# Performance work log

Measured on AMD Instinct MI355X. Metric: run time of the kernel, lower is better.

The kernel has to match this reference:

```python
import jax, jax.numpy as jnp
import numpy as np

B, N, D, E, FF_MULT = 2, 1024, 1024, 8, 4
H = D * FF_MULT


def setup_inputs() -> dict:
    key = jax.random.key(0)
    k = jax.random.split(key, 6)
    tokens = jax.random.normal(k[0], (B, N, D), dtype=jnp.float32)
    # uniform(0,1): strictly positive -> every expert processes every token
    dispatch_weights = jax.random.uniform(k[1], (B, N, E), dtype=jnp.float32)
    combine_weights = jax.random.uniform(k[2], (B, N, E), dtype=jnp.float32)
    # per-expert SwiGLU params, stacked on leading expert axis.
    # stored pre-transposed: y = x @ W  (torch Linear weight is [out,in])
    xavier_dh = np.sqrt(2.0 / (D + H))
    Wg = jax.random.normal(k[3], (E, D, H), dtype=jnp.float32) * xavier_dh
    Wv = jax.random.normal(k[4], (E, D, H), dtype=jnp.float32) * xavier_dh
    Wo = jax.random.normal(k[5], (E, H, D), dtype=jnp.float32) * (0.02 * xavier_dh)
    scale = jnp.full((E,), 1.0 / E, dtype=jnp.float32)  # output_scale init 1/E
    return {"tokens": tokens, "dispatch_weights": dispatch_weights,
            "combine_weights": combine_weights, "Wg": Wg, "Wv": Wv,
            "Wo": Wo, "scale": scale}


def reference(tokens, dispatch_weights, combine_weights, Wg, Wv, Wo, scale):
    b, n, d = tokens.shape
    x = tokens.reshape(b * n, d)                      # (T, D)
    disp = dispatch_weights.reshape(b * n, E)         # (T, E)
    comb = combine_weights.reshape(b * n, E)          # (T, E)
    # SwiGLU FFN for all experts at once (dense grouped GEMM)
    gate = jax.nn.gelu(jnp.einsum('td,edh->teh', x, Wg), approximate=False)
    value = jnp.einsum('td,edh->teh', x, Wv)
    expert_out = jnp.einsum('teh,ehd->ted', gate * value, Wo)  # (T, E, D)
    expert_out = expert_out * scale[None, :, None]
    # combine: weight by combine_weights where dispatched (dispatch > 0)
    w = jnp.where(disp > 0, comb, 0.0)                # (T, E)
    output = jnp.einsum('ted,te->td', expert_out, w)
    return output.reshape(b, n, d)
```

## Files before the change

kernel.cpp:

```cpp
#include <hip/hip_runtime.h>
#include <math.h>

#define T_TOK 2048
#define DDIM 1024
#define HDIM 4096
#define NEXP 8
#define NPRIME 8192
#define KTOT (NEXP * HDIM)
#define NSPLIT 4

typedef unsigned short u16;
typedef __attribute__((ext_vector_type(4))) float f32x4;
typedef __attribute__((ext_vector_type(8))) __bf16 bf16x8;
typedef __attribute__((ext_vector_type(8))) unsigned short u16x8;
typedef __attribute__((ext_vector_type(4))) unsigned short u16x4;

__device__ __forceinline__ u16 f2bf(float f) {
  unsigned int u = __builtin_bit_cast(unsigned int, f);
  u += 0x7fffu + ((u >> 16) & 1u);
  return (u16)(u >> 16);
}

__device__ __forceinline__ void stage16(const u16* g, u16* l) {
  __builtin_amdgcn_global_load_lds((__attribute__((address_space(1))) void*)g,
                                   (__attribute__((address_space(3))) void*)l,
                                   16, 0, 0);
}

__global__ void cvt_x_kernel(const float* __restrict__ x, u16* __restrict__ xb) {
  int i = (blockIdx.x * 256 + threadIdx.x) * 8;
  float4 a = *(const float4*)(x + i);
  float4 b = *(const float4*)(x + i + 4);
  u16x8 o;
  o[0] = f2bf(a.x); o[1] = f2bf(a.y); o[2] = f2bf(a.z); o[3] = f2bf(a.w);
  o[4] = f2bf(b.x); o[5] = f2bf(b.y); o[6] = f2bf(b.z); o[7] = f2bf(b.w);
  *(u16x8*)(xb + i) = o;
}

__global__ void transpose_all_kernel(const float* __restrict__ Wg,
                                     const float* __restrict__ Wv,
                                     const float* __restrict__ Wo,
                                     u16* __restrict__ wgvT, u16* __restrict__ woT2) {
  __shared__ float lds[64][65];
  const int bid = blockIdx.x;
  const int e = bid / 3072;
  const int r = bid % 3072;
  const int which = r >> 10;
  const int tt = r & 1023;
  const float* src; int R, C;
  if (which == 2) { src = Wo + (size_t)e * HDIM * DDIM; R = HDIM; C = DDIM; }
  else            { src = (which ? Wv : Wg) + (size_t)e * DDIM * HDIM; R = DDIM; C = HDIM; }
  const int nrt = R >> 6;
  const int r0 = (tt % nrt) << 6, c0 = (tt / nrt) << 6;
  const int tid = threadIdx.x;
#pragma unroll
  for (int i = 0; i < 4; ++i) {
    int f4 = tid + 256 * i;
    int row = f4 >> 4, c4 = (f4 & 15) << 2;
    float4 v = *(const float4*)(src + (size_t)(r0 + row) * C + c0 + c4);
    lds[row][c4] = v.x; lds[row][c4 + 1] = v.y; lds[row][c4 + 2] = v.z; lds[row][c4 + 3] = v.w;
  }
  __syncthreads();
#pragma unroll
  for (int i = 0; i < 4; ++i) {
    int f4 = tid + 256 * i;
    int cc = f4 >> 4, r4 = (f4 & 15) << 2;
    u16x4 o;
    o[0] = f2bf(lds[r4][cc]);     o[1] = f2bf(lds[r4 + 1][cc]);
    o[2] = f2bf(lds[r4 + 2][cc]); o[3] = f2bf(lds[r4 + 3][cc]);
    u16* dst;
    if (which == 2) {
      dst = woT2 + (size_t)(c0 + cc) * KTOT + e * HDIM + r0 + r4;
    } else {
      int h = c0 + cc;
      int rowp = ((h >> 4) << 5) + which * 16 + (h & 15);
      dst = wgvT + (size_t)e * NPRIME * DDIM + (size_t)rowp * DDIM + r0 + r4;
    }
    *(u16x4*)dst = o;
  }
}


__global__ void __launch_bounds__(512, 2)
gemm_gv_kernel(const u16* __restrict__ xb, const u16* __restrict__ wgvT,
               const float* __restrict__ disp, const float* __restrict__ comb,
               const float* __restrict__ scale, u16* __restrict__ h) {
  __shared__ u16 lds[3 * 24576];

  const int bid = blockIdx.x;
  const int wg = (bid & 7) * 512 + (bid >> 3);
  const int e  = wg >> 9;
  const int nt = (wg >> 3) & 63;
  const int mt = wg & 7;

  const int tid = threadIdx.x;
  const int lane = tid & 63;
  const int wave = tid >> 6;
  const int wr = wave >> 1;
  const int wc = wave & 1;
  const int l15 = lane & 15;
  const int lkq = lane >> 4;

  const u16* Ag = xb;
  const u16* Bg = wgvT + (size_t)e * NPRIME * DDIM;
  const int Am0 = mt * 256;
  const int Bn0 = nt * 128;

  const u16* gsrc[6];
  int ldst[6];
#pragma unroll
  for (int i = 0; i < 6; ++i) {
    int c = tid + 512 * i;
    if (c < 2048) { int row = c >> 3, sl = c & 7;
      gsrc[i] = Ag + (size_t)(Am0 + row) * DDIM + ((sl ^ (row & 7)) << 3);
    } else { int cb = c - 2048, row = cb >> 3, sl = cb & 7;
      gsrc[i] = Bg + (size_t)(Bn0 + row) * DDIM + ((sl ^ (row & 7)) << 3);
    }
    ldst[i] = c << 3;
  }
  auto STAGE = [&](int t) {
    const int k0 = t << 6;
    u16* lb = lds + (t % 3) * 24576;
#pragma unroll
    for (int i = 0; i < 6; ++i) stage16(gsrc[i] + k0, lb + ldst[i]);
  };

  f32x4 acc[4][4] = {};
  const int NT = DDIM / 64;

  STAGE(0); STAGE(1);
  asm volatile("s_waitcnt vmcnt(6)" ::: "memory");
  __builtin_amdgcn_s_barrier();

  for (int t = 0; t < NT; ++t) {
    if (t + 2 < NT) STAGE(t + 2);
    const u16* lb = lds + (t % 3) * 24576;
    bf16x8 af[2][4], bf[2][4];
#pragma unroll
    for (int ks = 0; ks < 2; ++ks) {
#pragma unroll
      for (int m = 0; m < 4; ++m) {
        int row = wr * 64 + m * 16 + l15;
        int sl = ((ks << 2) | lkq) ^ (row & 7);
        af[ks][m] = *(const bf16x8*)&lb[row * 64 + (sl << 3)];
      }
#pragma unroll
      for (int n = 0; n < 4; ++n) {
        int row = wc * 64 + n * 16 + l15;
        int sl = ((ks << 2) | lkq) ^ (row & 7);
        bf[ks][n] = *(const bf16x8*)&lb[16384 + row * 64 + (sl << 3)];
      }
    }
    __builtin_amdgcn_s_setprio(1);
#pragma unroll
    for (int ks = 0; ks < 2; ++ks)
#pragma unroll
      for (int m = 0; m < 4; ++m)
#pragma unroll
        for (int n = 0; n < 4; ++n)
          acc[m][n] = __builtin_amdgcn_mfma_f32_16x16x32_bf16(af[ks][m], bf[ks][n], acc[m][n], 0, 0, 0);
    __builtin_amdgcn_s_setprio(0);
    if (t < NT - 1) {
      asm volatile("s_waitcnt lgkmcnt(0)" ::: "memory");
      __builtin_amdgcn_sched_barrier(0);
      if (t + 2 < NT) asm volatile("s_waitcnt vmcnt(6)" ::: "memory");
      else            asm volatile("s_waitcnt vmcnt(0)" ::: "memory");
      __builtin_amdgcn_s_barrier();
    }
  }

  const float s_e = scale[e];
  const int hcb = nt * 64 + wc * 32;
#pragma unroll
  for (int m = 0; m < 4; ++m) {
#pragma unroll
    for (int r = 0; r < 4; ++r) {
      const int t = Am0 + wr * 64 + m * 16 + lkq * 4 + r;
      const float dv = disp[t * NEXP + e];
      const float cv = comb[t * NEXP + e];
      const float s = (dv > 0.0f) ? cv * s_e : 0.0f;
#pragma unroll
      for (int j = 0; j < 2; ++j) {
        const float g = acc[m][2 * j][r];
        const float v = acc[m][2 * j + 1][r];
        const float ge = 0.5f * g * (1.0f + erff(g * 0.70710678f));
        h[(size_t)t * KTOT + e * HDIM + hcb + j * 16 + l15] = f2bf(ge * v * s);
      }
    }
  }
}

__global__ void __launch_bounds__(512, 2)
gemm_out_kernel(const u16* __restrict__ hb, const u16* __restrict__ woT2,
                float* __restrict__ P) {
  __shared__ u16 lds[3 * 24576];

  const int bid = blockIdx.x;
  const int wg = (bid & 7) * 32 + (bid >> 3);
  const int kz = wg >> 6;
  const int nt = (wg >> 3) & 7;
  const int mt = wg & 7;

  const int tid = threadIdx.x;
  const int lane = tid & 63;
  const int wave = tid >> 6;
  const int wr = wave >> 1;
  const int wc = wave & 1;
  const int l15 = lane & 15;
  const int lkq = lane >> 4;

  const int Am0 = mt * 256;
  const int Bn0 = nt * 128;
  const int kbase = kz * (KTOT / NSPLIT);

  const u16* gsrc[6];
  int ldst[6];
#pragma unroll
  for (int i = 0; i < 6; ++i) {
    int c = tid + 512 * i;
    if (c < 2048) { int row = c >> 3, sl = c & 7;
      gsrc[i] = hb + (size_t)(Am0 + row) * KTOT + kbase + ((sl ^ (row & 7)) << 3);
    } else { int cb = c - 2048, row = cb >> 3, sl = cb & 7;
      gsrc[i] = woT2 + (size_t)(Bn0 + row) * KTOT + kbase + ((sl ^ (row & 7)) << 3);
    }
    ldst[i] = c << 3;
  }
  auto STAGE = [&](int t) {
    const int k0 = t << 6;
    u16* lb = lds + (t % 3) * 24576;
#pragma unroll
    for (int i = 0; i < 6; ++i) stage16(gsrc[i] + k0, lb + ldst[i]);
  };

  f32x4 acc[4][4] = {};
  const int NT = (KTOT / NSPLIT) / 64;

  STAGE(0); STAGE(1);
  asm volatile("s_waitcnt vmcnt(6)" ::: "memory");
  __builtin_amdgcn_s_barrier();

  for (int t = 0; t < NT; ++t) {
    if (t + 2 < NT) STAGE(t + 2);
    const u16* lb = lds + (t % 3) * 24576;
    bf16x8 af[2][4], bf[2][4];
#pragma unroll
    for (int ks = 0; ks < 2; ++ks) {
#pragma unroll
      for (int m = 0; m < 4; ++m) {
        int row = wr * 64 + m * 16 + l15;
        int sl = ((ks << 2) | lkq) ^ (row & 7);
        af[ks][m] = *(const bf16x8*)&lb[row * 64 + (sl << 3)];
      }
#pragma unroll
      for (int n = 0; n < 4; ++n) {
        int row = wc * 64 + n * 16 + l15;
        int sl = ((ks << 2) | lkq) ^ (row & 7);
        bf[ks][n] = *(const bf16x8*)&lb[16384 + row * 64 + (sl << 3)];
      }
    }
    __builtin_amdgcn_s_setprio(1);
#pragma unroll
    for (int ks = 0; ks < 2; ++ks)
#pragma unroll
      for (int m = 0; m < 4; ++m)
#pragma unroll
        for (int n = 0; n < 4; ++n)
          acc[m][n] = __builtin_amdgcn_mfma_f32_16x16x32_bf16(af[ks][m], bf[ks][n], acc[m][n], 0, 0, 0);
    __builtin_amdgcn_s_setprio(0);
    if (t < NT - 1) {
      asm volatile("s_waitcnt lgkmcnt(0)" ::: "memory");
      __builtin_amdgcn_sched_barrier(0);
      if (t + 2 < NT) asm volatile("s_waitcnt vmcnt(6)" ::: "memory");
      else            asm volatile("s_waitcnt vmcnt(0)" ::: "memory");
      __builtin_amdgcn_s_barrier();
    }
  }

  float* Pp = P + (size_t)kz * (T_TOK * DDIM);
#pragma unroll
  for (int m = 0; m < 4; ++m) {
#pragma unroll
    for (int r = 0; r < 4; ++r) {
      const int t = Am0 + wr * 64 + m * 16 + lkq * 4 + r;
#pragma unroll
      for (int n = 0; n < 4; ++n)
        Pp[(size_t)t * DDIM + Bn0 + wc * 64 + n * 16 + l15] = acc[m][n][r];
    }
  }
}

__global__ void reduce_out_kernel(const float* __restrict__ P, float* __restrict__ out) {
  int i = blockIdx.x * 256 + threadIdx.x;
  float4 a = ((const float4*)P)[i];
#pragma unroll
  for (int s = 1; s < NSPLIT; ++s) {
    float4 b = ((const float4*)P)[i + s * (T_TOK * DDIM / 4)];
    a.x += b.x; a.y += b.y; a.z += b.z; a.w += b.w;
  }
  ((float4*)out)[i] = a;
}

extern "C" void kernel_launch(void* const* d_in, const int* in_sizes, int n_in,
                              void* d_out, int out_size, void* d_ws, size_t ws_size,
                              hipStream_t stream) {
  const float* tokens = (const float*)d_in[0];
  const float* disp   = (const float*)d_in[1];
  const float* comb   = (const float*)d_in[2];
  const float* Wg     = (const float*)d_in[3];
  const float* Wv     = (const float*)d_in[4];
  const float* Wo     = (const float*)d_in[5];
  const float* scale  = (const float*)d_in[6];
  float* out = (float*)d_out;

  char* ws = (char*)d_ws;
  const size_t MB = 1024 * 1024;
  u16* xb    = (u16*)(ws);
  u16* wgvT  = (u16*)(ws + 4   * MB);
  u16* woT2  = (u16*)(ws + 132 * MB);
  u16* hbuf  = (u16*)(ws + 196 * MB);
  float* P   = (float*)(ws + 324 * MB);

  cvt_x_kernel<<<1024, 256, 0, stream>>>(tokens, xb);
  transpose_all_kernel<<<24576, 256, 0, stream>>>(Wg, Wv, Wo, wgvT, woT2);
  gemm_gv_kernel<<<4096, 512, 0, stream>>>(xb, wgvT, disp, comb, scale, hbuf);
  gemm_out_kernel<<<256, 512, 0, stream>>>(hbuf, woT2, P);
  reduce_out_kernel<<<2048, 256, 0, stream>>>(P, out);
}
```

Before: 589.5 us.

## Enlarge GEMM tiles to 256x256 with interleaved half-tile double-buffered staging

Both GEMM kernels now share a templated main loop that computes 256x256 output tiles with 8 waves in a 2x4 layout. Each wave holds 8x4 accumulator fragments, which raises data reuse per LDS load. The three-stage LDS ring is replaced by two 64 KB slots, with the A tile staged in halves and interleaved between MFMA phases and barriers. The gate/value GEMM grid is halved to match, and the output GEMM split-K goes from 4 to 8 to keep its block count. The trade-offs are higher register pressure, more barriers per iteration, a larger split-K partial buffer and extra reduction traffic.

```diff
diff --git a/kernel.cpp b/kernel.cpp
--- a/kernel.cpp
+++ b/kernel.cpp
@@ -7,7 +7,7 @@
 #define NEXP 8
 #define NPRIME 8192
 #define KTOT (NEXP * HDIM)
-#define NSPLIT 4
+#define NSPLIT 8
 
 typedef unsigned short u16;
 typedef __attribute__((ext_vector_type(4))) float f32x4;
@@ -81,110 +81,165 @@
 }
 
 
+template<int KS>
+__device__ __forceinline__ void stageA_half(const u16* Ab, int Am0, int tk,
+                                            u16* slot, int tid, int h) {
+#pragma unroll
+  for (int i = 0; i < 2; ++i) {
+    int ca = tid + i * 512;
+    int rowi = ca >> 3, sl = ca & 7;
+    int row = (rowi & 63) + h * 64 + (rowi >> 6) * 128;
+    const u16* g = Ab + (size_t)(Am0 + row) * KS + tk + ((sl ^ (row & 7)) << 3);
+    stage16(g, slot + ((row << 3) + sl) * 8);
+  }
+}
+template<int KS>
+__device__ __forceinline__ void stageB_full(const u16* Bb, int Bn0, int tk,
+                                            u16* slot, int tid) {
+#pragma unroll
+  for (int i = 0; i < 4; ++i) {
+    int cb = tid + i * 512;
+    int row = cb >> 3, sl = cb & 7;
+    const u16* g = Bb + (size_t)(Bn0 + row) * KS + tk + ((sl ^ (row & 7)) << 3);
+    stage16(g, slot + 16384 + cb * 8);
+  }
+}
+
+__device__ __forceinline__ bf16x8 ldsA(const u16* slot, int row, int j, int lkq) {
+  int sl = ((j << 2) | lkq) ^ (row & 7);
+  return *(const bf16x8*)(slot + row * 64 + sl * 8);
+}
+__device__ __forceinline__ bf16x8 ldsB(const u16* slot, int row, int j, int lkq) {
+  int sl = ((j << 2) | lkq) ^ (row & 7);
+  return *(const bf16x8*)(slot + 16384 + row * 64 + sl * 8);
+}
+
+template<int KS>
+__device__ __forceinline__ void gemm_loop(const u16* Ab, const u16* Bb,
+                                          int Am0, int Bn0, int kbase, int NT,
+                                          u16* lds, int tid, f32x4 (&acc)[8][4]) {
+  const int lane = tid & 63;
+  const int wave = tid >> 6;
+  const int wm = wave >> 2;
+  const int wn = wave & 3;
+  const int l15 = lane & 15;
+  const int lkq = lane >> 4;
+
+  u16* slot0 = lds;
+  u16* slot1 = lds + 32768;
+
+  stageA_half<KS>(Ab, Am0, kbase, slot0, tid, 0);
+  stageA_half<KS>(Ab, Am0, kbase, slot0, tid, 1);
+  stageB_full<KS>(Bb, Bn0, kbase, slot0, tid);
+  stageA_half<KS>(Ab, Am0, kbase + 64, slot1, tid, 0);
+  asm volatile("s_waitcnt vmcnt(2)" ::: "memory");
+  asm volatile("s_barrier" ::: "memory");
+
+#pragma unroll 1
+  for (int t = 0; t < NT; ++t) {
+    u16* s  = lds + (t & 1) * 32768;
+    u16* s2 = lds + ((t & 1) ^ 1) * 32768;
+    bf16x8 af[4], bfr[2][4];
+
+    if (t + 1 < NT) {
+      stageA_half<KS>(Ab, Am0, kbase + (t + 1) * 64, s2, tid, 1);
+      stageB_full<KS>(Bb, Bn0, kbase + (t + 1) * 64, s2, tid);
+    }
+#pragma unroll
+    for (int mf = 0; mf < 4; ++mf) af[mf] = ldsA(s, wm * 128 + mf * 16 + l15, 0, lkq);
+#pragma unroll
+    for (int nf = 0; nf < 4; ++nf) bfr[0][nf] = ldsB(s, wn * 64 + nf * 16 + l15, 0, lkq);
+    __builtin_amdgcn_s_setprio(1);
+#pragma unroll
+    for (int mf = 0; mf < 4; ++mf)
+#pragma unroll
+      for (int nf = 0; nf < 4; ++nf)
+        acc[mf][nf] = __builtin_amdgcn_mfma_f32_16x16x32_bf16(af[mf], bfr[0][nf], acc[mf][nf], 0, 0, 0);
+    __builtin_amdgcn_s_setprio(0);
+    asm volatile("s_barrier" ::: "memory");
+
+#pragma unroll
+    for (int mf = 0; mf < 4; ++mf) af[mf] = ldsA(s, wm * 128 + 64 + mf * 16 + l15, 0, lkq);
+    __builtin_amdgcn_s_setprio(1);
+#pragma unroll
+    for (int mf = 0; mf < 4; ++mf)
+#pragma unroll
+      for (int nf = 0; nf < 4; ++nf)
+        acc[4 + mf][nf] = __builtin_amdgcn_mfma_f32_16x16x32_bf16(af[mf], bfr[0][nf], acc[4 + mf][nf], 0, 0, 0);
+    __builtin_amdgcn_s_setprio(0);
+    asm volatile("s_barrier" ::: "memory");
+
+#pragma unroll
+    for (int mf = 0; mf < 4; ++mf) af[mf] = ldsA(s, wm * 128 + mf * 16 + l15, 1, lkq);
+#pragma unroll
+    for (int nf = 0; nf < 4; ++nf) bfr[1][nf] = ldsB(s, wn * 64 + nf * 16 + l15, 1, lkq);
+    __builtin_amdgcn_s_setprio(1);
+#pragma unroll
+    for (int mf = 0; mf < 4; ++mf)
+#pragma unroll
+      for (int nf = 0; nf < 4; ++nf)
+        acc[mf][nf] = __builtin_amdgcn_mfma_f32_16x16x32_bf16(af[mf], bfr[1][nf], acc[mf][nf], 0, 0, 0);
+    __builtin_amdgcn_s_setprio(0);
+    asm volatile("s_barrier" ::: "memory");
+
+    if (t + 2 < NT) stageA_half<KS>(Ab, Am0, kbase + (t + 2) * 64, s, tid, 0);
+#pragma unroll
+    for (int mf = 0; mf < 4; ++mf) af[mf] = ldsA(s, wm * 128 + 64 + mf * 16 + l15, 1, lkq);
+    __builtin_amdgcn_s_setprio(1);
+#pragma unroll
+    for (int mf = 0; mf < 4; ++mf)
+#pragma unroll
+      for (int nf = 0; nf < 4; ++nf)
+        acc[4 + mf][nf] = __builtin_amdgcn_mfma_f32_16x16x32_bf16(af[mf], bfr[1][nf], acc[4 + mf][nf], 0, 0, 0);
+    __builtin_amdgcn_s_setprio(0);
+    if (t + 2 < NT)       { asm volatile("s_waitcnt vmcnt(2)" ::: "memory"); }
+    else if (t + 2 == NT) { asm volatile("s_waitcnt vmcnt(0)" ::: "memory"); }
+    asm volatile("s_barrier" ::: "memory");
+  }
+}
+
 __global__ void __launch_bounds__(512, 2)
 gemm_gv_kernel(const u16* __restrict__ xb, const u16* __restrict__ wgvT,
                const float* __restrict__ disp, const float* __restrict__ comb,
                const float* __restrict__ scale, u16* __restrict__ h) {
-  __shared__ u16 lds[3 * 24576];
+  __shared__ u16 lds[65536];
 
   const int bid = blockIdx.x;
-  const int wg = (bid & 7) * 512 + (bid >> 3);
-  const int e  = wg >> 9;
-  const int nt = (wg >> 3) & 63;
-  const int mt = wg & 7;
+  const int wg = (bid & 7) * 256 + (bid >> 3);
+  const int e  = wg >> 8;
+  const int rr = wg & 255;
+  const int nt = rr >> 3;
+  const int mt = rr & 7;
 
   const int tid = threadIdx.x;
   const int lane = tid & 63;
   const int wave = tid >> 6;
-  const int wr = wave >> 1;
-  const int wc = wave & 1;
-  const int l15 = lane & 15;
-  const int lkq = lane >> 4;
-
-  const u16* Ag = xb;
-  const u16* Bg = wgvT + (size_t)e * NPRIME * DDIM;
+  const int wm = wave >> 2, wn = wave & 3;
+  const int l15 = lane & 15, lkq = lane >> 4;
+
+  const u16* Bb = wgvT + (size_t)e * NPRIME * DDIM;
   const int Am0 = mt * 256;
-  const int Bn0 = nt * 128;
-
-  const u16* gsrc[6];
-  int ldst[6];
-#pragma unroll
-  for (int i = 0; i < 6; ++i) {
-    int c = tid + 512 * i;
-    if (c < 2048) { int row = c >> 3, sl = c & 7;
-      gsrc[i] = Ag + (size_t)(Am0 + row) * DDIM + ((sl ^ (row & 7)) << 3);
-    } else { int cb = c - 2048, row = cb >> 3, sl = cb & 7;
-      gsrc[i] = Bg + (size_t)(Bn0 + row) * DDIM + ((sl ^ (row & 7)) << 3);
-    }
-    ldst[i] = c << 3;
-  }
-  auto STAGE = [&](int t) {
-    const int k0 = t << 6;
-    u16* lb = lds + (t % 3) * 24576;
-#pragma unroll
-    for (int i = 0; i < 6; ++i) stage16(gsrc[i] + k0, lb + ldst[i]);
-  };
-
-  f32x4 acc[4][4] = {};
-  const int NT = DDIM / 64;
-
-  STAGE(0); STAGE(1);
-  asm volatile("s_waitcnt vmcnt(6)" ::: "memory");
-  __builtin_amdgcn_s_barrier();
-
-  for (int t = 0; t < NT; ++t) {
-    if (t + 2 < NT) STAGE(t + 2);
-    const u16* lb = lds + (t % 3) * 24576;
-    bf16x8 af[2][4], bf[2][4];
-#pragma unroll
-    for (int ks = 0; ks < 2; ++ks) {
-#pragma unroll
-      for (int m = 0; m < 4; ++m) {
-        int row = wr * 64 + m * 16 + l15;
-        int sl = ((ks << 2) | lkq) ^ (row & 7);
-        af[ks][m] = *(const bf16x8*)&lb[row * 64 + (sl << 3)];
-      }
-#pragma unroll
-      for (int n = 0; n < 4; ++n) {
-        int row = wc * 64 + n * 16 + l15;
-        int sl = ((ks << 2) | lkq) ^ (row & 7);
-        bf[ks][n] = *(const bf16x8*)&lb[16384 + row * 64 + (sl << 3)];
-      }
-    }
-    __builtin_amdgcn_s_setprio(1);
-#pragma unroll
-    for (int ks = 0; ks < 2; ++ks)
-#pragma unroll
-      for (int m = 0; m < 4; ++m)
-#pragma unroll
-        for (int n = 0; n < 4; ++n)
-          acc[m][n] = __builtin_amdgcn_mfma_f32_16x16x32_bf16(af[ks][m], bf[ks][n], acc[m][n], 0, 0, 0);
-    __builtin_amdgcn_s_setprio(0);
-    if (t < NT - 1) {
-      asm volatile("s_waitcnt lgkmcnt(0)" ::: "memory");
-      __builtin_amdgcn_sched_barrier(0);
-      if (t + 2 < NT) asm volatile("s_waitcnt vmcnt(6)" ::: "memory");
-      else            asm volatile("s_waitcnt vmcnt(0)" ::: "memory");
-      __builtin_amdgcn_s_barrier();
-    }
-  }
+  const int Bn0 = nt * 256;
+
+  f32x4 acc[8][4] = {};
+  gemm_loop<DDIM>(xb, Bb, Am0, Bn0, 0, DDIM / 64, lds, tid, acc);
 
   const float s_e = scale[e];
-  const int hcb = nt * 64 + wc * 32;
-#pragma unroll
-  for (int m = 0; m < 4; ++m) {
+  const int hbase = nt * 128 + wn * 32;
+#pragma unroll
+  for (int a = 0; a < 8; ++a) {
 #pragma unroll
     for (int r = 0; r < 4; ++r) {
-      const int t = Am0 + wr * 64 + m * 16 + lkq * 4 + r;
+      const int t = Am0 + wm * 128 + a * 16 + lkq * 4 + r;
       const float dv = disp[t * NEXP + e];
       const float cv = comb[t * NEXP + e];
       const float s = (dv > 0.0f) ? cv * s_e : 0.0f;
 #pragma unroll
-      for (int j = 0; j < 2; ++j) {
-        const float g = acc[m][2 * j][r];
-        const float v = acc[m][2 * j + 1][r];
+      for (int jj = 0; jj < 2; ++jj) {
+        const float g = acc[a][2 * jj][r];
+        const float v = acc[a][2 * jj + 1][r];
         const float ge = 0.5f * g * (1.0f + erff(g * 0.70710678f));
-        h[(size_t)t * KTOT + e * HDIM + hcb + j * 16 + l15] = f2bf(ge * v * s);
+        h[(size_t)t * KTOT + e * HDIM + hbase + jj * 16 + l15] = f2bf(ge * v * s);
       }
     }
   }
@@ -193,98 +248,37 @@
 __global__ void __launch_bounds__(512, 2)
 gemm_out_kernel(const u16* __restrict__ hb, const u16* __restrict__ woT2,
                 float* __restrict__ P) {
-  __shared__ u16 lds[3 * 24576];
+  __shared__ u16 lds[65536];
 
   const int bid = blockIdx.x;
   const int wg = (bid & 7) * 32 + (bid >> 3);
-  const int kz = wg >> 6;
-  const int nt = (wg >> 3) & 7;
-  const int mt = wg & 7;
+  const int kz = wg >> 5;
+  const int rr = wg & 31;
+  const int nt = rr >> 3;
+  const int mt = rr & 7;
 
   const int tid = threadIdx.x;
   const int lane = tid & 63;
   const int wave = tid >> 6;
-  const int wr = wave >> 1;
-  const int wc = wave & 1;
-  const int l15 = lane & 15;
-  const int lkq = lane >> 4;
+  const int wm = wave >> 2, wn = wave & 3;
+  const int l15 = lane & 15, lkq = lane >> 4;
 
   const int Am0 = mt * 256;
-  const int Bn0 = nt * 128;
+  const int Bn0 = nt * 256;
   const int kbase = kz * (KTOT / NSPLIT);
 
-  const u16* gsrc[6];
-  int ldst[6];
-#pragma unroll
-  for (int i = 0; i < 6; ++i) {
-    int c = tid + 512 * i;
-    if (c < 2048) { int row = c >> 3, sl = c & 7;
-      gsrc[i] = hb + (size_t)(Am0 + row) * KTOT + kbase + ((sl ^ (row & 7)) << 3);
-    } else { int cb = c - 2048, row = cb >> 3, sl = cb & 7;
-      gsrc[i] = woT2 + (size_t)(Bn0 + row) * KTOT + kbase + ((sl ^ (row & 7)) << 3);
-    }
-    ldst[i] = c << 3;
-  }
-  auto STAGE = [&](int t) {
-    const int k0 = t << 6;
-    u16* lb = lds + (t % 3) * 24576;
-#pragma unroll
-    for (int i = 0; i < 6; ++i) stage16(gsrc[i] + k0, lb + ldst[i]);
-  };
-
-  f32x4 acc[4][4] = {};
-  const int NT = (KTOT / NSPLIT) / 64;
-
-  STAGE(0); STAGE(1);
-  asm volatile("s_waitcnt vmcnt(6)" ::: "memory");
-  __builtin_amdgcn_s_barrier();
-
-  for (int t = 0; t < NT; ++t) {
-    if (t + 2 < NT) STAGE(t + 2);
-    const u16* lb = lds + (t % 3) * 24576;
-    bf16x8 af[2][4], bf[2][4];
-#pragma unroll
-    for (int ks = 0; ks < 2; ++ks) {
-#pragma unroll
-      for (int m = 0; m < 4; ++m) {
-        int row = wr * 64 + m * 16 + l15;
-        int sl = ((ks << 2) | lkq) ^ (row & 7);
-        af[ks][m] = *(const bf16x8*)&lb[row * 64 + (sl << 3)];
-      }
-#pragma unroll
-      for (int n = 0; n < 4; ++n) {
-        int row = wc * 64 + n * 16 + l15;
-        int sl = ((ks << 2) | lkq) ^ (row & 7);
-        bf[ks][n] = *(const bf16x8*)&lb[16384 + row * 64 + (sl << 3)];
-      }
-    }
-    __builtin_amdgcn_s_setprio(1);
-#pragma unroll
-    for (int ks = 0; ks < 2; ++ks)
-#pragma unroll
-      for (int m = 0; m < 4; ++m)
-#pragma unroll
-        for (int n = 0; n < 4; ++n)
-          acc[m][n] = __builtin_amdgcn_mfma_f32_16x16x32_bf16(af[ks][m], bf[ks][n], acc[m][n], 0, 0, 0);
-    __builtin_amdgcn_s_setprio(0);
-    if (t < NT - 1) {
-      asm volatile("s_waitcnt lgkmcnt(0)" ::: "memory");
-      __builtin_amdgcn_sched_barrier(0);
-      if (t + 2 < NT) asm volatile("s_waitcnt vmcnt(6)" ::: "memory");
-      else            asm volatile("s_waitcnt vmcnt(0)" ::: "memory");
-      __builtin_amdgcn_s_barrier();
-    }
-  }
+  f32x4 acc[8][4] = {};
+  gemm_loop<KTOT>(hb, woT2, Am0, Bn0, kbase, (KTOT / NSPLIT) / 64, lds, tid, acc);
 
   float* Pp = P + (size_t)kz * (T_TOK * DDIM);
 #pragma unroll
-  for (int m = 0; m < 4; ++m) {
+  for (int a = 0; a < 8; ++a) {
 #pragma unroll
     for (int r = 0; r < 4; ++r) {
-      const int t = Am0 + wr * 64 + m * 16 + lkq * 4 + r;
-#pragma unroll
-      for (int n = 0; n < 4; ++n)
-        Pp[(size_t)t * DDIM + Bn0 + wc * 64 + n * 16 + l15] = acc[m][n][r];
+      const int t = Am0 + wm * 128 + a * 16 + lkq * 4 + r;
+#pragma unroll
+      for (int nf = 0; nf < 4; ++nf)
+        Pp[(size_t)t * DDIM + Bn0 + wn * 64 + nf * 16 + l15] = acc[a][nf][r];
     }
   }
 }
@@ -322,7 +316,7 @@
 
   cvt_x_kernel<<<1024, 256, 0, stream>>>(tokens, xb);
   transpose_all_kernel<<<24576, 256, 0, stream>>>(Wg, Wv, Wo, wgvT, woT2);
-  gemm_gv_kernel<<<4096, 512, 0, stream>>>(xb, wgvT, disp, comb, scale, hbuf);
+  gemm_gv_kernel<<<2048, 512, 0, stream>>>(xb, wgvT, disp, comb, scale, hbuf);
   gemm_out_kernel<<<256, 512, 0, stream>>>(hbuf, woT2, P);
   reduce_out_kernel<<<2048, 256, 0, stream>>>(P, out);
 }
```

Result: faster. 555.3 us (-5.8%).
